# Optimization experiments

Measured on AMD Instinct MI355X. Metric: run time of the kernel, lower is better.

The kernel has to match this reference:

```python
import jax, jax.numpy as jnp
import numpy as np
from jax import lax

KERNEL_SIZE = 11
SIGMA = 1.5
C1 = 0.01 ** 2
C2 = 0.03 ** 2


def _gaussian_kernel(channels):
    x = np.arange(KERNEL_SIZE, dtype=np.float32) - (KERNEL_SIZE // 2)
    g = np.exp(-(x ** 2) / (2.0 * SIGMA ** 2))
    g = g / g.sum()
    k2 = np.outer(g, g).astype(np.float32)  # (k, k)
    # depthwise weight layout OIHW with I=1, O=channels
    return jnp.asarray(np.broadcast_to(k2, (channels, 1, KERNEL_SIZE, KERNEL_SIZE)))


def _blur(x, kernel):
    # depthwise gaussian conv, SAME padding (padding = k//2, odd kernel, stride 1)
    return lax.conv_general_dilated(
        x, kernel,
        window_strides=(1, 1),
        padding='SAME',
        dimension_numbers=('NCHW', 'OIHW', 'NCHW'),
        feature_group_count=x.shape[1],
    )


def setup_inputs() -> dict:
    key = jax.random.key(0)
    k1, k2 = jax.random.split(key)
    img1 = jax.random.uniform(k1, (16, 3, 512, 512), dtype=jnp.float32)
    img2 = jax.random.uniform(k2, (16, 3, 512, 512), dtype=jnp.float32)
    return {"img1": img1, "img2": img2}


def reference(img1, img2):
    kernel = _gaussian_kernel(img1.shape[1]).astype(img1.dtype)
    mu1 = _blur(img1, kernel)
    mu2 = _blur(img2, kernel)
    mu1_sq = mu1 * mu1
    mu2_sq = mu2 * mu2
    mu1_mu2 = mu1 * mu2
    sigma1_sq = _blur(img1 * img1, kernel) - mu1_sq
    sigma2_sq = _blur(img2 * img2, kernel) - mu2_sq
    sigma12 = _blur(img1 * img2, kernel) - mu1_mu2
    ssim_map = ((2 * mu1_mu2 + C1) * (2 * sigma12 + C2)) / (
        (mu1_sq + mu2_sq + C1) * (sigma1_sq + sigma2_sq + C2))
    return jnp.mean(ssim_map)
```

## Files before the change

### kernel.cpp

```cpp
#include <hip/hip_runtime.h>
#include <math.h>

#define WIDTH   512
#define NPLANE  48
#define TILE    32
#define HALO    5
#define NROWS   42
#define SSTR    52
#define HBS     44
#define GRIDX   16
#define NBLOCKS (GRIDX*GRIDX*NPLANE)
#define NPIX    (16.0*3.0*512.0*512.0)

struct GaussW { float w[11]; };

union SU {
    float s[2][NROWS][SSTR];
    float hb[5 * 32 * HBS];
};

__device__ __forceinline__ void blur16(const float* vin, const GaussW& gw, float* o)
{
    #pragma unroll
    for (int t = 0; t < 16; ++t) {
        float s = vin[t] * gw.w[0];
        #pragma unroll
        for (int k = 1; k < 11; ++k) s = fmaf(gw.w[k], vin[t + k], s);
        o[t] = s;
    }
}

__global__ __launch_bounds__(256, 5)
void ssim_tile_kernel(const float* __restrict__ img1,
                      const float* __restrict__ img2,
                      float* __restrict__ partial, GaussW gw)
{
    __shared__ __align__(16) SU su;
    __shared__ float red[4];

    const int tid = threadIdx.x;
    const int bx = blockIdx.x, by = blockIdx.y, bz = blockIdx.z;
    const float* __restrict__ p1 = img1 + (size_t)bz * (WIDTH * WIDTH);
    const float* __restrict__ p2 = img2 + (size_t)bz * (WIDTH * WIDTH);
    const int gx0 = bx * TILE - 8;
    const int gy0 = by * TILE - HALO;

    const bool interior = ((unsigned)(bx - 1) < 14u) & ((unsigned)(by - 1) < 14u);

    if (interior) {
        #pragma unroll
        for (int k = 0; k < 4; ++k) {
            int l = tid + (k << 8);
            if (l < 1008) {
                int img = l >= 504;
                int u2  = img ? l - 504 : l;
                int r   = u2 / 12;
                int p   = u2 - r * 12;
                const float* gp = (img ? p2 : p1) + (gy0 + r) * WIDTH + (gx0 + (p << 2));
                *(float4*)&su.s[img][r][p << 2] = *(const float4*)gp;
            }
        }
    } else {
        #pragma unroll
        for (int k = 0; k < 4; ++k) {
            int l = tid + (k << 8);
            if (l < 1008) {
                int img = l >= 504;
                int u2  = img ? l - 504 : l;
                int r   = u2 / 12;
                int p   = u2 - r * 12;
                int gr = gy0 + r, gc = gx0 + (p << 2);
                float4 v = make_float4(0.f, 0.f, 0.f, 0.f);
                if ((unsigned)gr < WIDTH && (unsigned)gc <= (WIDTH - 4))
                    v = *(const float4*)((img ? p2 : p1) + gr * WIDTH + gc);
                *(float4*)&su.s[img][r][p << 2] = v;
            }
        }
    }
    __syncthreads();

    const bool active = tid < 252;
    float oa[16], ob[16];
    int qa = 0, qb = 0, r = 0, c0 = 0, g = 0;
    if (active) {
        g = (tid >= 84) + (tid >= 168);
        int u2 = tid - g * 84;
        r  = u2 >> 1;
        c0 = (u2 & 1) << 4;
        float ld[32];
        if (g < 2) {
            const float* sp = &su.s[g][r][c0];
            #pragma unroll
            for (int p = 0; p < 8; ++p) {
                float4 v = *(const float4*)(sp + (p << 2));
                ld[4*p] = v.x; ld[4*p+1] = v.y; ld[4*p+2] = v.z; ld[4*p+3] = v.w;
            }
            blur16(ld + 3, gw, oa);
            #pragma unroll
            for (int i = 0; i < 26; ++i) ld[3 + i] *= ld[3 + i];
            blur16(ld + 3, gw, ob);
            qa = g; qb = g + 2;
        } else {
            float lb[32];
            const float* spa = &su.s[0][r][c0];
            const float* spb = &su.s[1][r][c0];
            #pragma unroll
            for (int p = 0; p < 8; ++p) {
                float4 v = *(const float4*)(spa + (p << 2));
                ld[4*p] = v.x; ld[4*p+1] = v.y; ld[4*p+2] = v.z; ld[4*p+3] = v.w;
                float4 w2 = *(const float4*)(spb + (p << 2));
                lb[4*p] = w2.x; lb[4*p+1] = w2.y; lb[4*p+2] = w2.z; lb[4*p+3] = w2.w;
            }
            #pragma unroll
            for (int i = 0; i < 26; ++i) ld[3 + i] *= lb[3 + i];
            blur16(ld + 3, gw, oa);
            qa = 4;
        }
    }
    __syncthreads();

    if (active) {
        const int ba = qa * 32 + c0;
        #pragma unroll
        for (int j = 0; j < 16; ++j)
            su.hb[(ba + j) * HBS + r] = oa[j];
        if (g < 2) {
            const int bb = qb * 32 + c0;
            #pragma unroll
            for (int j = 0; j < 16; ++j)
                su.hb[(bb + j) * HBS + r] = ob[j];
        }
    }
    __syncthreads();

    const int c  = tid & 31;
    const int r0 = (tid >> 5) << 2;
    float acc[5][4];
    #pragma unroll
    for (int q = 0; q < 5; ++q) {
        const int base = (q * 32 + c) * HBS + r0;
        float win[16];
        #pragma unroll
        for (int k = 0; k < 4; ++k) {
            float4 v = *(const float4*)&su.hb[base + (k << 2)];
            win[4*k] = v.x; win[4*k+1] = v.y; win[4*k+2] = v.z; win[4*k+3] = v.w;
        }
        #pragma unroll
        for (int i = 0; i < 4; ++i) {
            float s = win[i] * gw.w[0];
            #pragma unroll
            for (int k = 1; k < 11; ++k) s = fmaf(gw.w[k], win[i + k], s);
            acc[q][i] = s;
        }
    }

    const float C1 = 0.01f * 0.01f, C2 = 0.03f * 0.03f;
    float ssum = 0.f;
    #pragma unroll
    for (int i = 0; i < 4; ++i) {
        float a = acc[0][i], b = acc[1][i];
        float ab = a * b, a2 = a * a, b2 = b * b;
        float s11 = acc[2][i] - a2;
        float s22 = acc[3][i] - b2;
        float s12 = acc[4][i] - ab;
        float num = (2.f * ab + C1) * (2.f * s12 + C2);
        float den = (a2 + b2 + C1) * (s11 + s22 + C2);
        ssum += num / den;
    }

    #pragma unroll
    for (int off = 32; off > 0; off >>= 1) ssum += __shfl_down(ssum, off);
    if ((tid & 63) == 0) red[tid >> 6] = ssum;
    __syncthreads();
    if (tid == 0)
        partial[bx + GRIDX * (by + GRIDX * bz)] = red[0] + red[1] + red[2] + red[3];
}

__global__ __launch_bounds__(1024)
void ssim_reduce_kernel(const float* __restrict__ partial, float* __restrict__ out)
{
    __shared__ double red[16];
    double s = 0.0;
    for (int i = threadIdx.x; i < NBLOCKS; i += 1024) s += (double)partial[i];
    #pragma unroll
    for (int off = 32; off > 0; off >>= 1) s += __shfl_down(s, off);
    if ((threadIdx.x & 63) == 0) red[threadIdx.x >> 6] = s;
    __syncthreads();
    if (threadIdx.x == 0) {
        double t = 0.0;
        #pragma unroll
        for (int w = 0; w < 16; ++w) t += red[w];
        out[0] = (float)(t / NPIX);
    }
}

extern "C" void kernel_launch(void* const* d_in, const int* in_sizes, int n_in,
                              void* d_out, int out_size, void* d_ws, size_t ws_size,
                              hipStream_t stream)
{
    GaussW gw;
    double g[11], sum = 0.0;
    for (int i = 0; i < 11; ++i) {
        double x = (double)(i - 5);
        g[i] = exp(-(x * x) / 4.5);
        sum += g[i];
    }
    for (int i = 0; i < 11; ++i) gw.w[i] = (float)(g[i] / sum);

    const float* img1 = (const float*)d_in[0];
    const float* img2 = (const float*)d_in[1];
    float* partial = (float*)d_ws;
    float* out = (float*)d_out;

    dim3 grid(GRIDX, GRIDX, NPLANE);
    hipLaunchKernelGGL(ssim_tile_kernel, grid, dim3(256), 0, stream,
                       img1, img2, partial, gw);
    hipLaunchKernelGGL(ssim_reduce_kernel, dim3(1), dim3(1024), 0, stream,
                       partial, out);
}
```

Measured before the change: 179.6 us.

## Load inputs directly from global into registers, enlarge tiles to 32x64

The horizontal blur pass now reads input rows straight from global memory into registers, so the staged input tile in shared memory is gone and one barrier is dropped. Tiles become 32 wide by 64 tall with 512 threads, which halves the vertical halo overhead per output pixel, and each thread now produces 8 outputs instead of 16. The SSIM division is replaced by a hardware reciprocal refined with one Newton step. The trade-offs are more global loads per thread, including scalar, non-coalesced loads on border tiles, and different occupancy and register pressure.

Result: slower. 302.0 us (+68.1%).

```diff
diff --git a/kernel.cpp b/kernel.cpp
--- a/kernel.cpp
+++ b/kernel.cpp
@@ -3,26 +3,21 @@
 
 #define WIDTH   512
 #define NPLANE  48
-#define TILE    32
-#define HALO    5
-#define NROWS   42
-#define SSTR    52
-#define HBS     44
-#define GRIDX   16
-#define NBLOCKS (GRIDX*GRIDX*NPLANE)
+#define TW      32
+#define TH      64
+#define SROWS   74
+#define HBS     76
+#define GX      16
+#define GY      8
+#define NBLOCKS (GX*GY*NPLANE)
 #define NPIX    (16.0*3.0*512.0*512.0)
 
 struct GaussW { float w[11]; };
 
-union SU {
-    float s[2][NROWS][SSTR];
-    float hb[5 * 32 * HBS];
-};
-
-__device__ __forceinline__ void blur16(const float* vin, const GaussW& gw, float* o)
-{
-    #pragma unroll
-    for (int t = 0; t < 16; ++t) {
+__device__ __forceinline__ void blur8(const float* vin, const GaussW& gw, float* o)
+{
+    #pragma unroll
+    for (int t = 0; t < 8; ++t) {
         float s = vin[t] * gw.w[0];
         #pragma unroll
         for (int k = 1; k < 11; ++k) s = fmaf(gw.w[k], vin[t + k], s);
@@ -30,105 +25,91 @@
     }
 }
 
-__global__ __launch_bounds__(256, 5)
+__global__ __launch_bounds__(512, 6)
 void ssim_tile_kernel(const float* __restrict__ img1,
                       const float* __restrict__ img2,
                       float* __restrict__ partial, GaussW gw)
 {
-    __shared__ __align__(16) SU su;
-    __shared__ float red[4];
+    __shared__ __align__(16) float hb[5 * TW * HBS];
+    __shared__ float red[8];
 
     const int tid = threadIdx.x;
     const int bx = blockIdx.x, by = blockIdx.y, bz = blockIdx.z;
     const float* __restrict__ p1 = img1 + (size_t)bz * (WIDTH * WIDTH);
     const float* __restrict__ p2 = img2 + (size_t)bz * (WIDTH * WIDTH);
-    const int gx0 = bx * TILE - 8;
-    const int gy0 = by * TILE - HALO;
-
-    const bool interior = ((unsigned)(bx - 1) < 14u) & ((unsigned)(by - 1) < 14u);
-
-    if (interior) {
-        #pragma unroll
-        for (int k = 0; k < 4; ++k) {
-            int l = tid + (k << 8);
-            if (l < 1008) {
-                int img = l >= 504;
-                int u2  = img ? l - 504 : l;
-                int r   = u2 / 12;
-                int p   = u2 - r * 12;
-                const float* gp = (img ? p2 : p1) + (gy0 + r) * WIDTH + (gx0 + (p << 2));
-                *(float4*)&su.s[img][r][p << 2] = *(const float4*)gp;
+    const int gx0 = bx * TW - 8;
+    const int gy0 = by * TH - 5;
+    const bool interior = ((unsigned)(bx - 1) < 14u) & ((unsigned)(by - 1) < 6u);
+
+    #pragma unroll
+    for (int round = 0; round < 2; ++round) {
+        int it = tid + (round << 9);
+        if (it < 888) {
+            int g   = it / 296;
+            int rem = it - g * 296;
+            int r   = rem >> 2;
+            int c0  = (rem & 3) << 3;
+            int grow  = gy0 + r;
+            int gcol0 = gx0 + c0;
+            float ld[24];
+            if (g < 2) {
+                const float* __restrict__ bp = (g ? p2 : p1);
+                if (interior) {
+                    const float* wp = bp + grow * WIDTH + gcol0;
+                    #pragma unroll
+                    for (int p = 0; p < 6; ++p) {
+                        float4 v = *(const float4*)(wp + (p << 2));
+                        ld[4*p] = v.x; ld[4*p+1] = v.y; ld[4*p+2] = v.z; ld[4*p+3] = v.w;
+                    }
+                } else {
+                    bool rok = (unsigned)grow < WIDTH;
+                    #pragma unroll
+                    for (int w = 0; w < 24; ++w) {
+                        int gc = gcol0 + w;
+                        ld[w] = (rok && (unsigned)gc < WIDTH) ? bp[grow * WIDTH + gc] : 0.f;
+                    }
+                }
+                float oa[8], ob[8];
+                blur8(ld + 3, gw, oa);
+                #pragma unroll
+                for (int i = 3; i < 21; ++i) ld[i] *= ld[i];
+                blur8(ld + 3, gw, ob);
+                const int qa = g * TW + c0, qb = (g + 2) * TW + c0;
+                #pragma unroll
+                for (int j = 0; j < 8; ++j) hb[(qa + j) * HBS + r] = oa[j];
+                #pragma unroll
+                for (int j = 0; j < 8; ++j) hb[(qb + j) * HBS + r] = ob[j];
+            } else {
+                float lb[24];
+                if (interior) {
+                    const float* wa = p1 + grow * WIDTH + gcol0;
+                    const float* wb = p2 + grow * WIDTH + gcol0;
+                    #pragma unroll
+                    for (int p = 0; p < 6; ++p) {
+                        float4 v = *(const float4*)(wa + (p << 2));
+                        ld[4*p] = v.x; ld[4*p+1] = v.y; ld[4*p+2] = v.z; ld[4*p+3] = v.w;
+                        float4 u = *(const float4*)(wb + (p << 2));
+                        lb[4*p] = u.x; lb[4*p+1] = u.y; lb[4*p+2] = u.z; lb[4*p+3] = u.w;
+                    }
+                } else {
+                    bool rok = (unsigned)grow < WIDTH;
+                    #pragma unroll
+                    for (int w = 0; w < 24; ++w) {
+                        int gc = gcol0 + w;
+                        bool ok = rok && (unsigned)gc < WIDTH;
+                        int idx = grow * WIDTH + gc;
+                        ld[w] = ok ? p1[idx] : 0.f;
+                        lb[w] = ok ? p2[idx] : 0.f;
+                    }
+                }
+                #pragma unroll
+                for (int i = 3; i < 21; ++i) ld[i] *= lb[i];
+                float oa[8];
+                blur8(ld + 3, gw, oa);
+                const int qa = 4 * TW + c0;
+                #pragma unroll
+                for (int j = 0; j < 8; ++j) hb[(qa + j) * HBS + r] = oa[j];
             }
-        }
-    } else {
-        #pragma unroll
-        for (int k = 0; k < 4; ++k) {
-            int l = tid + (k << 8);
-            if (l < 1008) {
-                int img = l >= 504;
-                int u2  = img ? l - 504 : l;
-                int r   = u2 / 12;
-                int p   = u2 - r * 12;
-                int gr = gy0 + r, gc = gx0 + (p << 2);
-                float4 v = make_float4(0.f, 0.f, 0.f, 0.f);
-                if ((unsigned)gr < WIDTH && (unsigned)gc <= (WIDTH - 4))
-                    v = *(const float4*)((img ? p2 : p1) + gr * WIDTH + gc);
-                *(float4*)&su.s[img][r][p << 2] = v;
-            }
-        }
-    }
-    __syncthreads();
-
-    const bool active = tid < 252;
-    float oa[16], ob[16];
-    int qa = 0, qb = 0, r = 0, c0 = 0, g = 0;
-    if (active) {
-        g = (tid >= 84) + (tid >= 168);
-        int u2 = tid - g * 84;
-        r  = u2 >> 1;
-        c0 = (u2 & 1) << 4;
-        float ld[32];
-        if (g < 2) {
-            const float* sp = &su.s[g][r][c0];
-            #pragma unroll
-            for (int p = 0; p < 8; ++p) {
-                float4 v = *(const float4*)(sp + (p << 2));
-                ld[4*p] = v.x; ld[4*p+1] = v.y; ld[4*p+2] = v.z; ld[4*p+3] = v.w;
-            }
-            blur16(ld + 3, gw, oa);
-            #pragma unroll
-            for (int i = 0; i < 26; ++i) ld[3 + i] *= ld[3 + i];
-            blur16(ld + 3, gw, ob);
-            qa = g; qb = g + 2;
-        } else {
-            float lb[32];
-            const float* spa = &su.s[0][r][c0];
-            const float* spb = &su.s[1][r][c0];
-            #pragma unroll
-            for (int p = 0; p < 8; ++p) {
-                float4 v = *(const float4*)(spa + (p << 2));
-                ld[4*p] = v.x; ld[4*p+1] = v.y; ld[4*p+2] = v.z; ld[4*p+3] = v.w;
-                float4 w2 = *(const float4*)(spb + (p << 2));
-                lb[4*p] = w2.x; lb[4*p+1] = w2.y; lb[4*p+2] = w2.z; lb[4*p+3] = w2.w;
-            }
-            #pragma unroll
-            for (int i = 0; i < 26; ++i) ld[3 + i] *= lb[3 + i];
-            blur16(ld + 3, gw, oa);
-            qa = 4;
-        }
-    }
-    __syncthreads();
-
-    if (active) {
-        const int ba = qa * 32 + c0;
-        #pragma unroll
-        for (int j = 0; j < 16; ++j)
-            su.hb[(ba + j) * HBS + r] = oa[j];
-        if (g < 2) {
-            const int bb = qb * 32 + c0;
-            #pragma unroll
-            for (int j = 0; j < 16; ++j)
-                su.hb[(bb + j) * HBS + r] = ob[j];
         }
     }
     __syncthreads();
@@ -138,11 +119,11 @@
     float acc[5][4];
     #pragma unroll
     for (int q = 0; q < 5; ++q) {
-        const int base = (q * 32 + c) * HBS + r0;
+        const int base = (q * TW + c) * HBS + r0;
         float win[16];
         #pragma unroll
         for (int k = 0; k < 4; ++k) {
-            float4 v = *(const float4*)&su.hb[base + (k << 2)];
+            float4 v = *(const float4*)&hb[base + (k << 2)];
             win[4*k] = v.x; win[4*k+1] = v.y; win[4*k+2] = v.z; win[4*k+3] = v.w;
         }
         #pragma unroll
@@ -165,15 +146,21 @@
         float s12 = acc[4][i] - ab;
         float num = (2.f * ab + C1) * (2.f * s12 + C2);
         float den = (a2 + b2 + C1) * (s11 + s22 + C2);
-        ssum += num / den;
+        float inv = __builtin_amdgcn_rcpf(den);
+        inv = inv * fmaf(-den, inv, 2.0f);
+        ssum = fmaf(num, inv, ssum);
     }
 
     #pragma unroll
     for (int off = 32; off > 0; off >>= 1) ssum += __shfl_down(ssum, off);
     if ((tid & 63) == 0) red[tid >> 6] = ssum;
     __syncthreads();
-    if (tid == 0)
-        partial[bx + GRIDX * (by + GRIDX * bz)] = red[0] + red[1] + red[2] + red[3];
+    if (tid == 0) {
+        float t = 0.f;
+        #pragma unroll
+        for (int w = 0; w < 8; ++w) t += red[w];
+        partial[bx + GX * (by + GY * bz)] = t;
+    }
 }
 
 __global__ __launch_bounds__(1024)
@@ -212,8 +199,8 @@
     float* partial = (float*)d_ws;
     float* out = (float*)d_out;
 
-    dim3 grid(GRIDX, GRIDX, NPLANE);
-    hipLaunchKernelGGL(ssim_tile_kernel, grid, dim3(256), 0, stream,
+    dim3 grid(GX, GY, NPLANE);
+    hipLaunchKernelGGL(ssim_tile_kernel, grid, dim3(512), 0, stream,
                        img1, img2, partial, gw);
     hipLaunchKernelGGL(ssim_reduce_kernel, dim3(1), dim3(1024), 0, stream,
                        partial, out);
```
